# Optimization experiments

Measured on AMD Instinct MI355X. Metric: run time of the kernel, lower is better.

Reference implementation:

```python
import jax, jax.numpy as jnp
import numpy as np

N_NODES = 100000   # dict_size / number of nodes
K_RPR = 128        # FLAGS.k_RPR: neighbors per node
FEAT_DIM = 128     # feature dim
NVEC = 200         # nodevec_dim (== pretrained embedding dim)
BATCH = 1024       # batchsize placeholder
NEG = 64           # FLAGS.neg_sample_size


def setup_inputs() -> dict:
    key = jax.random.key(0)
    ks = jax.random.split(key, 9)
    return {
        "train_inputs": jax.random.randint(ks[0], (BATCH,), 0, N_NODES, dtype=jnp.int64 if jax.config.jax_enable_x64 else jnp.int32).astype(jnp.int32),
        "train_labels": jax.random.randint(ks[1], (BATCH,), 0, N_NODES).astype(jnp.int32),
        "neg_samples": jax.random.randint(ks[2], (NEG,), 0, N_NODES).astype(jnp.int32),
        "rpr_arg": jax.random.randint(ks[3], (N_NODES, K_RPR), 0, N_NODES).astype(jnp.int32),
        "rpr_matrix": jax.random.uniform(ks[4], (N_NODES, K_RPR), dtype=jnp.float32),
        "features": jax.random.normal(ks[5], (N_NODES, FEAT_DIM), dtype=jnp.float32),
        "embeddings": 0.1 * jax.random.normal(ks[6], (N_NODES, NVEC), dtype=jnp.float32),
        "nce_weights": 0.1 * jax.random.normal(ks[7], (N_NODES, NVEC), dtype=jnp.float32),
        "agg_W": (1.0 / np.sqrt(FEAT_DIM)) * jax.random.normal(ks[8], (FEAT_DIM, NVEC), dtype=jnp.float32),
    }


def _log_sig(x):
    # tf.log(tf.sigmoid(x) + 0.001)
    return jnp.log(jax.nn.sigmoid(x) + 0.001)


def _sample_aggregate(idx, rpr_arg, rpr_matrix, features, agg_W):
    # gather RPR neighbor ids and weights, then gather neighbor features
    nbr = rpr_arg[idx]              # [B, K]
    w = rpr_matrix[idx]             # [B, K]
    f = features[nbr]               # [B, K, F]
    agg = jnp.einsum('bk,bkf->bf', w, f)   # weighted aggregation over K neighbors
    return jax.nn.relu(agg @ agg_W)         # [B, NVEC] (WeightedAggregator dense+relu)


def reference(train_inputs, train_labels, neg_samples, rpr_arg, rpr_matrix,
              features, embeddings, nce_weights, agg_W):
    inf = _sample_aggregate(train_inputs, rpr_arg, rpr_matrix, features, agg_W)
    lf = _sample_aggregate(train_labels, rpr_arg, rpr_matrix, features, agg_W)
    nf = _sample_aggregate(neg_samples, rpr_arg, rpr_matrix, features, agg_W)

    embed = embeddings[train_inputs]    # [B, NVEC]
    true_w = nce_weights[train_labels]  # [B, NVEC]
    false_w = nce_weights[neg_samples]  # [NEG, NVEC]

    rho1, rho2, rho3 = 1.5, 0.75, 1.5
    p1 = _log_sig(jnp.sum(inf * lf, axis=1))          # [B]
    p2 = _log_sig(-jnp.sum(inf @ nf.T))                # scalar
    p3 = _log_sig(jnp.sum(embed * true_w, axis=1))
    p4 = _log_sig(-jnp.sum(embed @ false_w.T))
    p5 = _log_sig(jnp.sum(embed * lf, axis=1))
    p6 = _log_sig(-jnp.sum(embed @ nf.T))
    p7 = _log_sig(jnp.sum(true_w * inf, axis=1))
    p8 = _log_sig(-jnp.sum(true_w @ nf.T))

    temp = rho1 * (p1 + p2) + rho2 * (p3 + p4) + rho3 * (p5 + p6) + rho3 * (p7 + p8)
    loss = -jnp.sum(temp) / jnp.asarray(train_inputs.shape[0], jnp.float32)
    return loss
```

## Files before the change

### kernel.cpp

```cpp
#include <hip/hip_runtime.h>

#define BATCH 1024
#define NEG 64
#define KNB 128
#define FD 128
#define NV 200
#define NSLAB 8
#define SUMW (5 * NV + 1)

__device__ __forceinline__ float log_sig(float x) {
    float s = 1.0f / (1.0f + expf(-x));
    return logf(s + 0.001f);
}

__global__ __launch_bounds__(512, 8) void fused_kernel(
    const int* __restrict__ ti, const int* __restrict__ tl, const int* __restrict__ ns,
    const int* __restrict__ rpr_arg, const float* __restrict__ rpr_mat,
    const float* __restrict__ feat, const float* __restrict__ W,
    const float* __restrict__ emb, const float* __restrict__ nce,
    float* __restrict__ sums)
{
    int b = blockIdx.x, t = threadIdx.x, lane = t & 63, w = t >> 6;
    bool pair = (b < BATCH);
    float* slab = sums + (size_t)(b & (NSLAB - 1)) * SUMW;

    __shared__ int   nbr_sh[256];
    __shared__ float w_sh[256];
    __shared__ float part[8][FD];
    __shared__ float agg_i[FD], agg_l[FD];
    __shared__ float red[4][8];

    if (pair) {
        if (t < 256) {
            int idx = (t < 128) ? ti[b] : tl[b];
            nbr_sh[t] = rpr_arg[(size_t)idx * KNB + (t & 127)];
            w_sh[t]   = rpr_mat[(size_t)idx * KNB + (t & 127)];
        }
    } else if (t < 128) {
        int idx = ns[b - BATCH];
        nbr_sh[t] = rpr_arg[(size_t)idx * KNB + t];
        w_sh[t]   = rpr_mat[(size_t)idx * KNB + t];
    }
    __syncthreads();

    float accX = 0.f, accY = 0.f;
    {
        int nb   = pair ? 4 : 2;
        int base = pair ? (w * 32) : (w * 16);
        for (int bb = 0; bb < nb; ++bb) {
            int k0 = base + bb * 8;
            float2 d[8]; float ww[8];
            #pragma unroll
            for (int j = 0; j < 8; ++j) {
                ww[j] = w_sh[k0 + j];
                d[j]  = *(const float2*)&feat[(size_t)(unsigned)nbr_sh[k0 + j] * FD + 2 * lane];
            }
            #pragma unroll
            for (int j = 0; j < 8; ++j) {
                accX += ww[j] * d[j].x;
                accY += ww[j] * d[j].y;
            }
        }
    }
    ((float2*)part[w])[lane] = make_float2(accX, accY);
    __syncthreads();

    if (pair) {
        if (t < FD)
            agg_i[t] = part[0][t] + part[1][t] + part[2][t] + part[3][t];
        else if (t < 2 * FD) {
            int u = t - FD;
            agg_l[u] = part[4][u] + part[5][u] + part[6][u] + part[7][u];
        }
    } else if (t < FD) {
        agg_i[t] = part[0][t] + part[1][t] + part[2][t] + part[3][t]
                 + part[4][t] + part[5][t] + part[6][t] + part[7][t];
    }
    __syncthreads();

    float pi = 0.f, pl = 0.f;
    if (t < NV) {
        if (pair) {
            #pragma unroll 8
            for (int f = 0; f < FD; ++f) {
                float wv = W[f * NV + t];
                pi += agg_i[f] * wv;
                pl += agg_l[f] * wv;
            }
            pl = fmaxf(pl, 0.f);
        } else {
            #pragma unroll 8
            for (int f = 0; f < FD; ++f)
                pi += agg_i[f] * W[f * NV + t];
        }
        pi = fmaxf(pi, 0.f);
    }

    if (pair) {
        float e = 0.f, tw = 0.f;
        if (t < NV) {
            e  = emb[(size_t)ti[b] * NV + t];
            tw = nce[(size_t)tl[b] * NV + t];
            atomicAdd(&slab[t], pi);
            atomicAdd(&slab[2 * NV + t], e);
            atomicAdd(&slab[3 * NV + t], tw);
        }
        float v0 = pi * pl;
        float v1 = e * tw;
        float v2 = e * pl;
        float v3 = tw * pi;
        #pragma unroll
        for (int o = 32; o > 0; o >>= 1) {
            v0 += __shfl_down(v0, o, 64);
            v1 += __shfl_down(v1, o, 64);
            v2 += __shfl_down(v2, o, 64);
            v3 += __shfl_down(v3, o, 64);
        }
        if (lane == 0) {
            red[0][w] = v0; red[1][w] = v1; red[2][w] = v2; red[3][w] = v3;
        }
        __syncthreads();
        if (t == 0) {
            float d1 = 0.f, d3 = 0.f, d5 = 0.f, d7 = 0.f;
            #pragma unroll
            for (int i = 0; i < 8; ++i) {
                d1 += red[0][i]; d3 += red[1][i]; d5 += red[2][i]; d7 += red[3][i];
            }
            float s = 1.5f * log_sig(d1) + 0.75f * log_sig(d3)
                    + 1.5f * log_sig(d5) + 1.5f * log_sig(d7);
            atomicAdd(&slab[5 * NV], s);
        }
    } else {
        if (t < NV) {
            atomicAdd(&slab[NV + t], pi);
            atomicAdd(&slab[4 * NV + t], nce[(size_t)ns[b - BATCH] * NV + t]);
        }
    }
}

__global__ __launch_bounds__(256) void final_kernel(
    const float* __restrict__ sums, float* __restrict__ out)
{
    int t = threadIdx.x;
    float a = 0.f, bb = 0.f, c = 0.f, d = 0.f;
    if (t < NV) {
        float si = 0.f, sn = 0.f, se = 0.f, st = 0.f, sf = 0.f;
        #pragma unroll
        for (int s = 0; s < NSLAB; ++s) {
            const float* p = sums + s * SUMW;
            si += p[t];          sn += p[NV + t];     se += p[2 * NV + t];
            st += p[3 * NV + t]; sf += p[4 * NV + t];
        }
        a  = si * sn;
        bb = se * sf;
        c  = se * sn;
        d  = st * sn;
    }
    __shared__ float red[4][4];
    #pragma unroll
    for (int o = 32; o > 0; o >>= 1) {
        a  += __shfl_down(a, o, 64);
        bb += __shfl_down(bb, o, 64);
        c  += __shfl_down(c, o, 64);
        d  += __shfl_down(d, o, 64);
    }
    if ((t & 63) == 0) {
        int w = t >> 6;
        red[0][w] = a; red[1][w] = bb; red[2][w] = c; red[3][w] = d;
    }
    __syncthreads();
    if (t == 0) {
        float d2 = red[0][0] + red[0][1] + red[0][2] + red[0][3];
        float d4 = red[1][0] + red[1][1] + red[1][2] + red[1][3];
        float d6 = red[2][0] + red[2][1] + red[2][2] + red[2][3];
        float d8 = red[3][0] + red[3][1] + red[3][2] + red[3][3];
        float lacc = 0.f;
        #pragma unroll
        for (int s = 0; s < NSLAB; ++s) lacc += sums[s * SUMW + 5 * NV];
        float total = lacc + (float)BATCH * (1.5f * log_sig(-d2) + 0.75f * log_sig(-d4)
                                           + 1.5f * log_sig(-d6) + 1.5f * log_sig(-d8));
        out[0] = -total / (float)BATCH;
    }
}

extern "C" void kernel_launch(void* const* d_in, const int* in_sizes, int n_in,
                              void* d_out, int out_size, void* d_ws, size_t ws_size,
                              hipStream_t stream) {
    const int*   ti      = (const int*)d_in[0];
    const int*   tl      = (const int*)d_in[1];
    const int*   ns      = (const int*)d_in[2];
    const int*   rpr_arg = (const int*)d_in[3];
    const float* rpr_mat = (const float*)d_in[4];
    const float* feat    = (const float*)d_in[5];
    const float* emb     = (const float*)d_in[6];
    const float* nce     = (const float*)d_in[7];
    const float* W       = (const float*)d_in[8];

    float* sums = (float*)d_ws;

    hipMemsetAsync(d_ws, 0, (size_t)NSLAB * SUMW * sizeof(float), stream);
    fused_kernel<<<BATCH + NEG, 512, 0, stream>>>(
        ti, tl, ns, rpr_arg, rpr_mat, feat, W, emb, nce, sums);
    final_kernel<<<1, 256, 0, stream>>>(sums, (float*)d_out);
}
```

Before: 41.56 us.

## Convert feature table to bf16 each call before gathering neighbors

Adds a conversion kernel that rewrites the whole 100000x128 fp32 feature table into a packed bf16 copy in workspace, and has the gather read 32-bit pairs instead of float2. The same kernel also zeroes the accumulation slabs, replacing the memset call. The aim is to halve the bytes moved by the random neighbor-feature gather. In exchange, every call now streams the full 51 MB table and writes a 25.6 MB copy, which is far more traffic than the roughly 1088x128 gathered rows, and aggregation accuracy drops to bf16.

After: 44.00 us. +5.9%, slower.

```diff
diff --git a/kernel.cpp b/kernel.cpp
--- a/kernel.cpp
+++ b/kernel.cpp
@@ -4,19 +4,41 @@
 #define NEG 64
 #define KNB 128
 #define FD 128
+#define FD2 (FD / 2)
 #define NV 200
 #define NSLAB 8
 #define SUMW (5 * NV + 1)
+#define NFEAT4 3200000
 
 __device__ __forceinline__ float log_sig(float x) {
     float s = 1.0f / (1.0f + expf(-x));
     return logf(s + 0.001f);
 }
 
+__device__ __forceinline__ unsigned bf16_rne(float x) {
+    unsigned b = __float_as_uint(x);
+    return (b + 0x7FFFu + ((b >> 16) & 1u)) >> 16;
+}
+
+__global__ __launch_bounds__(256) void convert_kernel(
+    const float4* __restrict__ f4, uint2* __restrict__ tb, float* __restrict__ sums)
+{
+    if (blockIdx.x == 0)
+        for (int i = threadIdx.x; i < NSLAB * SUMW; i += 256) sums[i] = 0.f;
+    int stride = gridDim.x * blockDim.x;
+    for (int i = blockIdx.x * blockDim.x + threadIdx.x; i < NFEAT4; i += stride) {
+        float4 v = f4[i];
+        uint2 o;
+        o.x = bf16_rne(v.x) | (bf16_rne(v.y) << 16);
+        o.y = bf16_rne(v.z) | (bf16_rne(v.w) << 16);
+        tb[i] = o;
+    }
+}
+
 __global__ __launch_bounds__(512, 8) void fused_kernel(
     const int* __restrict__ ti, const int* __restrict__ tl, const int* __restrict__ ns,
     const int* __restrict__ rpr_arg, const float* __restrict__ rpr_mat,
-    const float* __restrict__ feat, const float* __restrict__ W,
+    const unsigned* __restrict__ tb, const float* __restrict__ W,
     const float* __restrict__ emb, const float* __restrict__ nce,
     float* __restrict__ sums)
 {
@@ -43,26 +65,26 @@
     }
     __syncthreads();
 
-    float accX = 0.f, accY = 0.f;
+    float accL = 0.f, accH = 0.f;
     {
         int nb   = pair ? 4 : 2;
         int base = pair ? (w * 32) : (w * 16);
         for (int bb = 0; bb < nb; ++bb) {
             int k0 = base + bb * 8;
-            float2 d[8]; float ww[8];
+            unsigned d[8]; float ww[8];
             #pragma unroll
             for (int j = 0; j < 8; ++j) {
                 ww[j] = w_sh[k0 + j];
-                d[j]  = *(const float2*)&feat[(size_t)(unsigned)nbr_sh[k0 + j] * FD + 2 * lane];
+                d[j]  = tb[(size_t)(unsigned)nbr_sh[k0 + j] * FD2 + lane];
             }
             #pragma unroll
             for (int j = 0; j < 8; ++j) {
-                accX += ww[j] * d[j].x;
-                accY += ww[j] * d[j].y;
-            }
-        }
-    }
-    ((float2*)part[w])[lane] = make_float2(accX, accY);
+                accL += ww[j] * __uint_as_float(d[j] << 16);
+                accH += ww[j] * __uint_as_float(d[j] & 0xFFFF0000u);
+            }
+        }
+    }
+    ((float2*)part[w])[lane] = make_float2(accL, accH);
     __syncthreads();
 
     if (pair) {
@@ -73,8 +95,10 @@
             agg_l[u] = part[4][u] + part[5][u] + part[6][u] + part[7][u];
         }
     } else if (t < FD) {
-        agg_i[t] = part[0][t] + part[1][t] + part[2][t] + part[3][t]
-                 + part[4][t] + part[5][t] + part[6][t] + part[7][t];
+        float s = 0.f;
+        #pragma unroll
+        for (int p = 0; p < 8; ++p) s += part[p][t];
+        agg_i[t] = s;
     }
     __syncthreads();
 
@@ -196,10 +220,12 @@
     const float* nce     = (const float*)d_in[7];
     const float* W       = (const float*)d_in[8];
 
-    float* sums = (float*)d_ws;
-
-    hipMemsetAsync(d_ws, 0, (size_t)NSLAB * SUMW * sizeof(float), stream);
+    float* ws = (float*)d_ws;
+    unsigned* tb = (unsigned*)ws;
+    float* sums  = ws + 6400000;
+
+    convert_kernel<<<2048, 256, 0, stream>>>((const float4*)feat, (uint2*)tb, sums);
     fused_kernel<<<BATCH + NEG, 512, 0, stream>>>(
-        ti, tl, ns, rpr_arg, rpr_mat, feat, W, emb, nce, sums);
+        ti, tl, ns, rpr_arg, rpr_mat, tb, W, emb, nce, sums);
     final_kernel<<<1, 256, 0, stream>>>(sums, (float*)d_out);
 }
```

## Replace slab atomics with per-row stores and a multi-block final reduction

Applied to the files above, without the earlier changes.

The per-element atomicAdds into eight shared slabs are replaced by plain transposed stores of each batch row's vectors into workspace, and the final kernel is spread over NV blocks that reduce columns, finishing with a last-block-done counter. The W projection is split across two halves of the block so 400 threads share the dot products. The memset is dropped because the fused kernel zeroes the small accumulator cells itself. This removes atomic contention and a launch, at the cost of more workspace traffic and a cross-kernel zeroing dependency.

New measurement: 65.83 us. 1.58x slower.

```diff
diff --git a/kernel.cpp b/kernel.cpp
--- a/kernel.cpp
+++ b/kernel.cpp
@@ -5,8 +5,14 @@
 #define KNB 128
 #define FD 128
 #define NV 200
-#define NSLAB 8
-#define SUMW (5 * NV + 1)
+
+#define O_INF  0
+#define O_EMB  (NV * BATCH)
+#define O_TW   (2 * NV * BATCH)
+#define O_LOSS (3 * NV * BATCH)
+#define O_NF   (3 * NV * BATCH + BATCH)
+#define O_FW   (3 * NV * BATCH + BATCH + NV * NEG)
+#define O_CELL (3 * NV * BATCH + BATCH + 2 * NV * NEG)
 
 __device__ __forceinline__ float log_sig(float x) {
     float s = 1.0f / (1.0f + expf(-x));
@@ -18,17 +24,19 @@
     const int* __restrict__ rpr_arg, const float* __restrict__ rpr_mat,
     const float* __restrict__ feat, const float* __restrict__ W,
     const float* __restrict__ emb, const float* __restrict__ nce,
-    float* __restrict__ sums)
+    float* __restrict__ ws)
 {
     int b = blockIdx.x, t = threadIdx.x, lane = t & 63, w = t >> 6;
     bool pair = (b < BATCH);
-    float* slab = sums + (size_t)(b & (NSLAB - 1)) * SUMW;
+
+    if (t < 6) ws[O_CELL + t] = 0.f;
 
     __shared__ int   nbr_sh[256];
     __shared__ float w_sh[256];
     __shared__ float part[8][FD];
     __shared__ float agg_i[FD], agg_l[FD];
-    __shared__ float red[4][8];
+    __shared__ float pB[NV], lB[NV];
+    __shared__ float red[4][4];
 
     if (pair) {
         if (t < 256) {
@@ -73,113 +81,133 @@
             agg_l[u] = part[4][u] + part[5][u] + part[6][u] + part[7][u];
         }
     } else if (t < FD) {
-        agg_i[t] = part[0][t] + part[1][t] + part[2][t] + part[3][t]
-                 + part[4][t] + part[5][t] + part[6][t] + part[7][t];
-    }
+        float s = 0.f;
+        #pragma unroll
+        for (int p = 0; p < 8; ++p) s += part[p][t];
+        agg_i[t] = s;
+    }
+    __syncthreads();
+
+    int g  = (t < NV) ? 0 : ((t >= 256 && t < 256 + NV) ? 1 : -1);
+    int tc = (g == 1) ? t - 256 : t;
+    float piH = 0.f, plH = 0.f;
+    if (g >= 0) {
+        int f0 = g * 64;
+        #pragma unroll 8
+        for (int f = f0; f < f0 + 64; ++f) {
+            float wv = W[f * NV + tc];
+            piH += agg_i[f] * wv;
+            if (pair) plH += agg_l[f] * wv;
+        }
+    }
+    if (g == 1) { pB[tc] = piH; lB[tc] = plH; }
     __syncthreads();
 
     float pi = 0.f, pl = 0.f;
-    if (t < NV) {
-        if (pair) {
-            #pragma unroll 8
-            for (int f = 0; f < FD; ++f) {
-                float wv = W[f * NV + t];
-                pi += agg_i[f] * wv;
-                pl += agg_l[f] * wv;
-            }
-            pl = fmaxf(pl, 0.f);
-        } else {
-            #pragma unroll 8
-            for (int f = 0; f < FD; ++f)
-                pi += agg_i[f] * W[f * NV + t];
-        }
-        pi = fmaxf(pi, 0.f);
+    if (g == 0) {
+        pi = fmaxf(piH + pB[t], 0.f);
+        pl = fmaxf(plH + lB[t], 0.f);
     }
 
     if (pair) {
         float e = 0.f, tw = 0.f;
-        if (t < NV) {
+        if (g == 0) {
             e  = emb[(size_t)ti[b] * NV + t];
             tw = nce[(size_t)tl[b] * NV + t];
-            atomicAdd(&slab[t], pi);
-            atomicAdd(&slab[2 * NV + t], e);
-            atomicAdd(&slab[3 * NV + t], tw);
-        }
-        float v0 = pi * pl;
-        float v1 = e * tw;
-        float v2 = e * pl;
-        float v3 = tw * pi;
-        #pragma unroll
-        for (int o = 32; o > 0; o >>= 1) {
-            v0 += __shfl_down(v0, o, 64);
-            v1 += __shfl_down(v1, o, 64);
-            v2 += __shfl_down(v2, o, 64);
-            v3 += __shfl_down(v3, o, 64);
-        }
-        if (lane == 0) {
-            red[0][w] = v0; red[1][w] = v1; red[2][w] = v2; red[3][w] = v3;
+            ws[O_INF + (size_t)t * BATCH + b] = pi;
+            ws[O_EMB + (size_t)t * BATCH + b] = e;
+            ws[O_TW  + (size_t)t * BATCH + b] = tw;
+        }
+        if (t < 256) {
+            float v0 = pi * pl;
+            float v1 = e * tw;
+            float v2 = e * pl;
+            float v3 = tw * pi;
+            #pragma unroll
+            for (int o = 32; o > 0; o >>= 1) {
+                v0 += __shfl_down(v0, o, 64);
+                v1 += __shfl_down(v1, o, 64);
+                v2 += __shfl_down(v2, o, 64);
+                v3 += __shfl_down(v3, o, 64);
+            }
+            if (lane == 0) {
+                red[0][w] = v0; red[1][w] = v1; red[2][w] = v2; red[3][w] = v3;
+            }
         }
         __syncthreads();
         if (t == 0) {
-            float d1 = 0.f, d3 = 0.f, d5 = 0.f, d7 = 0.f;
-            #pragma unroll
-            for (int i = 0; i < 8; ++i) {
-                d1 += red[0][i]; d3 += red[1][i]; d5 += red[2][i]; d7 += red[3][i];
-            }
-            float s = 1.5f * log_sig(d1) + 0.75f * log_sig(d3)
-                    + 1.5f * log_sig(d5) + 1.5f * log_sig(d7);
-            atomicAdd(&slab[5 * NV], s);
-        }
-    } else {
-        if (t < NV) {
-            atomicAdd(&slab[NV + t], pi);
-            atomicAdd(&slab[4 * NV + t], nce[(size_t)ns[b - BATCH] * NV + t]);
-        }
+            float d1 = red[0][0] + red[0][1] + red[0][2] + red[0][3];
+            float d3 = red[1][0] + red[1][1] + red[1][2] + red[1][3];
+            float d5 = red[2][0] + red[2][1] + red[2][2] + red[2][3];
+            float d7 = red[3][0] + red[3][1] + red[3][2] + red[3][3];
+            ws[O_LOSS + b] = 1.5f * log_sig(d1) + 0.75f * log_sig(d3)
+                           + 1.5f * log_sig(d5) + 1.5f * log_sig(d7);
+        }
+    } else if (g == 0) {
+        int nb_ = b - BATCH;
+        ws[O_NF + (size_t)t * NEG + nb_] = pi;
+        ws[O_FW + (size_t)t * NEG + nb_] = nce[(size_t)ns[nb_] * NV + t];
     }
 }
 
 __global__ __launch_bounds__(256) void final_kernel(
-    const float* __restrict__ sums, float* __restrict__ out)
+    float* __restrict__ ws, float* __restrict__ out)
 {
-    int t = threadIdx.x;
-    float a = 0.f, bb = 0.f, c = 0.f, d = 0.f;
-    if (t < NV) {
-        float si = 0.f, sn = 0.f, se = 0.f, st = 0.f, sf = 0.f;
-        #pragma unroll
-        for (int s = 0; s < NSLAB; ++s) {
-            const float* p = sums + s * SUMW;
-            si += p[t];          sn += p[NV + t];     se += p[2 * NV + t];
-            st += p[3 * NV + t]; sf += p[4 * NV + t];
-        }
-        a  = si * sn;
-        bb = se * sf;
-        c  = se * sn;
-        d  = st * sn;
-    }
-    __shared__ float red[4][4];
+    int t = blockIdx.x, tid = threadIdx.x, lane = tid & 63, w = tid >> 6;
+    const float* Ai = ws + O_INF + (size_t)t * BATCH;
+    const float* Ae = ws + O_EMB + (size_t)t * BATCH;
+    const float* At = ws + O_TW  + (size_t)t * BATCH;
+    float si = 0.f, se = 0.f, st = 0.f;
+    for (int i = tid; i < BATCH; i += 256) { si += Ai[i]; se += Ae[i]; st += At[i]; }
+    float sn = 0.f, sf = 0.f;
+    if (tid < NEG) {
+        sn = ws[O_NF + t * NEG + tid];
+        sf = ws[O_FW + t * NEG + tid];
+    }
+    float lp = 0.f;
+    if (tid < 6) {
+        int j = t + NV * tid;
+        if (j < BATCH) lp = ws[O_LOSS + j];
+    }
+
+    __shared__ float red[6][4];
     #pragma unroll
     for (int o = 32; o > 0; o >>= 1) {
-        a  += __shfl_down(a, o, 64);
-        bb += __shfl_down(bb, o, 64);
-        c  += __shfl_down(c, o, 64);
-        d  += __shfl_down(d, o, 64);
-    }
-    if ((t & 63) == 0) {
-        int w = t >> 6;
-        red[0][w] = a; red[1][w] = bb; red[2][w] = c; red[3][w] = d;
-    }
-    __syncthreads();
-    if (t == 0) {
-        float d2 = red[0][0] + red[0][1] + red[0][2] + red[0][3];
-        float d4 = red[1][0] + red[1][1] + red[1][2] + red[1][3];
-        float d6 = red[2][0] + red[2][1] + red[2][2] + red[2][3];
-        float d8 = red[3][0] + red[3][1] + red[3][2] + red[3][3];
-        float lacc = 0.f;
+        si += __shfl_down(si, o, 64); se += __shfl_down(se, o, 64);
+        st += __shfl_down(st, o, 64); sn += __shfl_down(sn, o, 64);
+        sf += __shfl_down(sf, o, 64); lp += __shfl_down(lp, o, 64);
+    }
+    if (lane == 0) {
+        red[0][w] = si; red[1][w] = se; red[2][w] = st;
+        red[3][w] = sn; red[4][w] = sf; red[5][w] = lp;
+    }
+    __syncthreads();
+    if (tid == 0) {
+        float Si = 0.f, Se = 0.f, St = 0.f, Sn = 0.f, Sf = 0.f, Lp = 0.f;
         #pragma unroll
-        for (int s = 0; s < NSLAB; ++s) lacc += sums[s * SUMW + 5 * NV];
-        float total = lacc + (float)BATCH * (1.5f * log_sig(-d2) + 0.75f * log_sig(-d4)
-                                           + 1.5f * log_sig(-d6) + 1.5f * log_sig(-d8));
-        out[0] = -total / (float)BATCH;
+        for (int i = 0; i < 4; ++i) {
+            Si += red[0][i]; Se += red[1][i]; St += red[2][i];
+            Sn += red[3][i]; Sf += red[4][i]; Lp += red[5][i];
+        }
+        float* c = ws + O_CELL;
+        atomicAdd(&c[0], Si * Sn);
+        atomicAdd(&c[1], Se * Sf);
+        atomicAdd(&c[2], Se * Sn);
+        atomicAdd(&c[3], St * Sn);
+        atomicAdd(&c[4], Lp);
+        __threadfence();
+        unsigned old = atomicAdd((unsigned*)&c[5], 1u);
+        if (old == NV - 1) {
+            float d2 = atomicAdd(&c[0], 0.f);
+            float d4 = atomicAdd(&c[1], 0.f);
+            float d6 = atomicAdd(&c[2], 0.f);
+            float d8 = atomicAdd(&c[3], 0.f);
+            float lacc = atomicAdd(&c[4], 0.f);
+            float total = lacc + (float)BATCH *
+                (1.5f * log_sig(-d2) + 0.75f * log_sig(-d4)
+               + 1.5f * log_sig(-d6) + 1.5f * log_sig(-d8));
+            out[0] = -total / (float)BATCH;
+        }
     }
 }
 
@@ -196,10 +224,9 @@
     const float* nce     = (const float*)d_in[7];
     const float* W       = (const float*)d_in[8];
 
-    float* sums = (float*)d_ws;
-
-    hipMemsetAsync(d_ws, 0, (size_t)NSLAB * SUMW * sizeof(float), stream);
+    float* ws = (float*)d_ws;
+
     fused_kernel<<<BATCH + NEG, 512, 0, stream>>>(
-        ti, tl, ns, rpr_arg, rpr_mat, feat, W, emb, nce, sums);
-    final_kernel<<<1, 256, 0, stream>>>(sums, (float*)d_out);
-}
+        ti, tl, ns, rpr_arg, rpr_mat, feat, W, emb, nce, ws);
+    final_kernel<<<NV, 256, 0, stream>>>(ws, (float*)d_out);
+}
```
